# Kernel optimization log

Measured on AMD Instinct MI355X. Metric: run time of the kernel, lower is better.

## Reference

```python
import jax, jax.numpy as jnp
import numpy as np

N, D_IN, D_OUT, B = 200000, 256, 256, 256

def setup_inputs() -> dict:
    key = jax.random.key(0)
    k1, k2, k3, k4, k5 = jax.random.split(key, 5)
    lim = float(np.sqrt(6.0 / (D_IN + D_OUT)))  # xavier_init scale=1
    return {
        "nodes": jax.random.normal(k1, (N, D_IN), dtype=jnp.float32),
        "owner_masks": jax.random.randint(k2, (B, N), 0, 2, dtype=jnp.int32),
        "Wt": jax.random.uniform(k3, (D_OUT, D_IN), jnp.float32, -lim, lim),
        "bt": jax.random.normal(k4, (D_OUT,), dtype=jnp.float32),
        "Wg": jax.random.uniform(k5, (D_OUT, D_IN), jnp.float32, -lim, lim),
        "bg": jnp.ones((D_OUT,), dtype=jnp.float32),  # gate bias init fill_(1)
    }

def reference(nodes, owner_masks, Wt, bt, Wg, bg):
    # gates = sigmoid(Linear(nodes)); data = Linear(nodes)  -> [N, D_OUT]
    gates = jax.nn.sigmoid(nodes @ Wg.T + bg)
    data = nodes @ Wt.T + bt
    # owner-mask matmul == masked scatter-sum over nodes -> [B, D_OUT]
    fmask = owner_masks.astype(jnp.float32)
    res = jnp.einsum('bn,nd->bd', fmask, data * gates)
    return res  # dropout is identity in eval mode
```

## Files before the change

### kernel.cpp

```cpp
#include <hip/hip_runtime.h>
#include <stdint.h>

#define NND 200000

typedef unsigned short u16;
typedef __attribute__((ext_vector_type(4))) float f4;
typedef __attribute__((ext_vector_type(4))) int   i4;
typedef __attribute__((ext_vector_type(2))) unsigned int u2;
typedef __attribute__((ext_vector_type(8))) short s8;
typedef __attribute__((ext_vector_type(4))) float acc4;

__device__ __forceinline__ short f2bf(float f) {
    union { float f; uint32_t u; } v; v.f = f;
    uint32_t r = v.u + 0x7FFFu + ((v.u >> 16) & 1u);
    return (short)(r >> 16);
}
__device__ __forceinline__ uint32_t pack2bf(float a, float b) {
    uint32_t ua = __float_as_uint(a), ub = __float_as_uint(b);
    ua = ua + 0x7FFFu + ((ua >> 16) & 1u);
    ub = ub + 0x7FFFu + ((ub >> 16) & 1u);
    return (ua >> 16) | (ub & 0xFFFF0000u);
}
__device__ __forceinline__ float bf2f(uint32_t s) { return __uint_as_float(s << 16); }
__device__ __forceinline__ void gld16(const void* g, void* l) {
    __builtin_amdgcn_global_load_lds(
        (const __attribute__((address_space(1))) void*)g,
        (__attribute__((address_space(3))) void*)l, 16, 0, 0);
}

__global__ __launch_bounds__(256) void k_prep(const float* __restrict__ Wt,
                                              const float* __restrict__ Wg,
                                              u16* __restrict__ wtb,
                                              u16* __restrict__ wgb) {
    int i = blockIdx.x * 256 + threadIdx.x;
    wtb[i] = (u16)f2bf(Wt[i]);
    wgb[i] = (u16)f2bf(Wg[i]);
}

__global__ __launch_bounds__(512, 4) void k_h(const float* __restrict__ nodes,
                                              const u16* __restrict__ wtb,
                                              const u16* __restrict__ wgb,
                                              const float* __restrict__ btp,
                                              const float* __restrict__ bgp,
                                              u16* __restrict__ h_t) {
    __shared__ __align__(16) char smem[74752];
    u16* Abf = (u16*)smem;
    u16* Ws  = (u16*)(smem + 9216);
    u16* Hs  = (u16*)smem;

    const int tid  = threadIdx.x;
    const int lane = tid & 63, wave = tid >> 6;
    const int quad = lane >> 4, l16 = lane & 15;
    const int n0 = blockIdx.x * 64;
    const int arow = tid >> 3, aslot = tid & 7;

    acc4 at_[4][2], ag_[4][2];
#pragma unroll
    for (int rt = 0; rt < 4; ++rt)
#pragma unroll
        for (int dt = 0; dt < 2; ++dt) { at_[rt][dt] = (acc4)0.0f; ag_[rt][dt] = (acc4)0.0f; }

    for (int kt = 0; kt < 4; ++kt) {
        const int k0 = kt * 64;
        const float* ap = nodes + (size_t)(n0 + arow) * 256 + k0 + aslot * 8;
        f4 a0 = ((const f4*)ap)[0];
        f4 a1 = ((const f4*)ap)[1];
        if (kt) __syncthreads();
#pragma unroll
        for (int i = 0; i < 4; ++i) {
            int g = i * 512 + tid;
            int dr = g >> 3, c = g & 7;
            size_t off = (size_t)dr * 256 + k0 + ((c ^ (dr & 7)) << 3);
            gld16(wtb + off, (char*)Ws + g * 16);
            gld16(wgb + off, (char*)Ws + 32768 + g * 16);
        }
        {
            i4 aw;
            aw.x = (int)pack2bf(a0.x, a0.y); aw.y = (int)pack2bf(a0.z, a0.w);
            aw.z = (int)pack2bf(a1.x, a1.y); aw.w = (int)pack2bf(a1.z, a1.w);
            *(i4*)((char*)Abf + arow * 144 + ((aslot ^ (arow & 7)) << 4)) = aw;
        }
        __syncthreads();
#pragma unroll
        for (int ks = 0; ks < 2; ++ks) {
            const int q = (ks << 2) | quad;
            s8 af[4];
#pragma unroll
            for (int rt = 0; rt < 4; ++rt)
                af[rt] = *(const s8*)((char*)Abf + (rt * 16 + l16) * 144 + ((q ^ (l16 & 7)) << 4));
#pragma unroll
            for (int dt = 0; dt < 2; ++dt) {
                int dl = wave * 32 + dt * 16 + l16;
                int sl = (q ^ (dl & 7)) << 4;
                s8 bT = *(const s8*)((char*)Ws + dl * 128 + sl);
                s8 bG = *(const s8*)((char*)Ws + 32768 + dl * 128 + sl);
#pragma unroll
                for (int rt = 0; rt < 4; ++rt) {
                    at_[rt][dt] = __builtin_amdgcn_mfma_f32_16x16x32_bf16(af[rt], bT, at_[rt][dt], 0, 0, 0);
                    ag_[rt][dt] = __builtin_amdgcn_mfma_f32_16x16x32_bf16(af[rt], bG, ag_[rt][dt], 0, 0, 0);
                }
            }
        }
    }
    __syncthreads();

#pragma unroll
    for (int dt = 0; dt < 2; ++dt) {
        int dl = wave * 32 + dt * 16 + l16;
        float btv = btp[dl], bgv = bgp[dl];
#pragma unroll
        for (int rt = 0; rt < 4; ++rt) {
            float h0 = (at_[rt][dt][0] + btv) / (1.0f + __expf(-(ag_[rt][dt][0] + bgv)));
            float h1 = (at_[rt][dt][1] + btv) / (1.0f + __expf(-(ag_[rt][dt][1] + bgv)));
            float h2 = (at_[rt][dt][2] + btv) / (1.0f + __expf(-(ag_[rt][dt][2] + bgv)));
            float h3 = (at_[rt][dt][3] + btv) / (1.0f + __expf(-(ag_[rt][dt][3] + bgv)));
            u2 p; p.x = pack2bf(h0, h1); p.y = pack2bf(h2, h3);
            *(u2*)((char*)Hs + dl * 144 + (rt * 16 + quad * 4) * 2) = p;
        }
    }
    __syncthreads();
#pragma unroll
    for (int i = 0; i < 4; ++i) {
        int g = i * 512 + tid;
        int d = g >> 3, c = g & 7;
        f4 v = *(const f4*)((char*)Hs + d * 144 + c * 16);
        *(f4*)(h_t + (size_t)d * NND + n0 + c * 8) = v;
    }
}

__global__ __launch_bounds__(512, 4) void k_res(const int* __restrict__ masks,
                                                const u16* __restrict__ h_t,
                                                float* __restrict__ outp) {
    __shared__ __align__(16) char smem[49152];
    u16* Ms = (u16*)smem;
    u16* Hs = (u16*)(smem + 16384);

    const int tid  = threadIdx.x;
    const int lane = tid & 63, wave = tid >> 6;
    const int quad = lane >> 4, l16 = lane & 15;
    const int bh = wave & 1, dq = wave >> 1;
    const int b0 = blockIdx.x * 128;
    const int nbase = blockIdx.y * 960;
    const int R = min(15, (NND - nbase) / 64);

    acc4 acc[4][4];
#pragma unroll
    for (int rt = 0; rt < 4; ++rt)
#pragma unroll
        for (int dt = 0; dt < 4; ++dt) acc[rt][dt] = (acc4)0.0f;

    const int mr0 = tid >> 3, mc0 = tid & 7;
    const int mr1 = (512 + tid) >> 3, mc1 = tid & 7;
    i4 mp[2][2];
    {
        const i4* p0 = (const i4*)(masks + (size_t)(b0 + mr0) * NND + nbase + mc0 * 8);
        const i4* p1 = (const i4*)(masks + (size_t)(b0 + mr1) * NND + nbase + mc1 * 8);
        mp[0][0] = p0[0]; mp[0][1] = p0[1];
        mp[1][0] = p1[0]; mp[1][1] = p1[1];
    }

    for (int it = 0; it < R; ++it) {
        const int nb = nbase + it * 64;
#pragma unroll
        for (int i = 0; i < 4; ++i) {
            int g = i * 512 + tid;
            int dr = g >> 3, c = g & 7;
            gld16(h_t + (size_t)dr * NND + nb + ((c ^ (dr & 7)) << 3), (char*)Hs + g * 16);
        }
#pragma unroll
        for (int i = 0; i < 2; ++i) {
            int mr = (i == 0) ? mr0 : mr1, c = (i == 0) ? mc0 : mc1;
            i4 w;
            w.x = (int)((((uint32_t)(-mp[i][0].x)) & 0x3F80u) | ((((uint32_t)(-mp[i][0].y)) & 0x3F80u) << 16));
            w.y = (int)((((uint32_t)(-mp[i][0].z)) & 0x3F80u) | ((((uint32_t)(-mp[i][0].w)) & 0x3F80u) << 16));
            w.z = (int)((((uint32_t)(-mp[i][1].x)) & 0x3F80u) | ((((uint32_t)(-mp[i][1].y)) & 0x3F80u) << 16));
            w.w = (int)((((uint32_t)(-mp[i][1].z)) & 0x3F80u) | ((((uint32_t)(-mp[i][1].w)) & 0x3F80u) << 16));
            *(i4*)((char*)Ms + mr * 128 + ((c ^ (mr & 7)) << 4)) = w;
        }
        __syncthreads();
        if (it + 1 < R) {
            const int nn = nb + 64;
            const i4* p0 = (const i4*)(masks + (size_t)(b0 + mr0) * NND + nn + mc0 * 8);
            const i4* p1 = (const i4*)(masks + (size_t)(b0 + mr1) * NND + nn + mc1 * 8);
            mp[0][0] = p0[0]; mp[0][1] = p0[1];
            mp[1][0] = p1[0]; mp[1][1] = p1[1];
        }
#pragma unroll
        for (int ks = 0; ks < 2; ++ks) {
            const int q = (ks << 2) | quad;
            s8 af[4];
#pragma unroll
            for (int rt = 0; rt < 4; ++rt) {
                int r = bh * 64 + rt * 16 + l16;
                af[rt] = *(const s8*)((char*)Ms + r * 128 + ((q ^ (l16 & 7)) << 4));
            }
#pragma unroll
            for (int dt = 0; dt < 4; ++dt) {
                int dl = dq * 64 + dt * 16 + l16;
                s8 bf_ = *(const s8*)((char*)Hs + dl * 128 + ((q ^ (dl & 7)) << 4));
#pragma unroll
                for (int rt = 0; rt < 4; ++rt)
                    acc[rt][dt] = __builtin_amdgcn_mfma_f32_16x16x32_bf16(af[rt], bf_, acc[rt][dt], 0, 0, 0);
            }
        }
        __syncthreads();
    }
#pragma unroll
    for (int rt = 0; rt < 4; ++rt)
#pragma unroll
        for (int dt = 0; dt < 4; ++dt) {
            int b = b0 + bh * 64 + rt * 16 + quad * 4;
            int d = dq * 64 + dt * 16 + l16;
#pragma unroll
            for (int r = 0; r < 4; ++r)
                atomicAdd(outp + (size_t)(b + r) * 256 + d, acc[rt][dt][r]);
        }
}

extern "C" void kernel_launch(void* const* d_in, const int* in_sizes, int n_in,
                              void* d_out, int out_size, void* d_ws, size_t ws_size,
                              hipStream_t stream) {
    const float* nodes = (const float*)d_in[0];
    const int*   masks = (const int*)d_in[1];
    const float* Wt    = (const float*)d_in[2];
    const float* bt    = (const float*)d_in[3];
    const float* Wg    = (const float*)d_in[4];
    const float* bg    = (const float*)d_in[5];
    float* outp = (float*)d_out;

    u16* h_t = (u16*)d_ws;
    u16* wtb = (u16*)((char*)d_ws + (size_t)102400000);
    u16* wgb = wtb + 65536;

    hipMemsetAsync(d_out, 0, (size_t)out_size * sizeof(float), stream);
    k_prep<<<dim3(256), dim3(256), 0, stream>>>(Wt, Wg, wtb, wgb);
    k_h<<<dim3(3125), dim3(512), 0, stream>>>(nodes, wtb, wgb, bt, bg, h_t);
    k_res<<<dim3(2, 209), dim3(512), 0, stream>>>(masks, h_t, outp);
}
```

Baseline: 502.2 us.

## Make k_h persistent with register-resident weights and double-buffered node chunks

Rewrites the gated linear kernel so each 1024-thread block keeps its slice of both bf16 weight matrices in registers for its whole life. Each block then streams 25 chunks of 32 nodes through double-buffered LDS, prefetching the next chunk's inputs and writing out the previous chunk's results while the current chunk runs its MFMAs. This drops the per-block reload of the full weight matrices and shrinks the grid from 3125 blocks to 250, which risks lower occupancy (250 blocks against the number of CUs) and higher register pressure from holding the weights.

```diff
diff --git a/kernel.cpp b/kernel.cpp
--- a/kernel.cpp
+++ b/kernel.cpp
@@ -21,7 +21,6 @@
     ub = ub + 0x7FFFu + ((ub >> 16) & 1u);
     return (ua >> 16) | (ub & 0xFFFF0000u);
 }
-__device__ __forceinline__ float bf2f(uint32_t s) { return __uint_as_float(s << 16); }
 __device__ __forceinline__ void gld16(const void* g, void* l) {
     __builtin_amdgcn_global_load_lds(
         (const __attribute__((address_space(1))) void*)g,
@@ -37,94 +36,100 @@
     wgb[i] = (u16)f2bf(Wg[i]);
 }
 
-__global__ __launch_bounds__(512, 4) void k_h(const float* __restrict__ nodes,
-                                              const u16* __restrict__ wtb,
-                                              const u16* __restrict__ wgb,
-                                              const float* __restrict__ btp,
-                                              const float* __restrict__ bgp,
-                                              u16* __restrict__ h_t) {
-    __shared__ __align__(16) char smem[74752];
-    u16* Abf = (u16*)smem;
-    u16* Ws  = (u16*)(smem + 9216);
-    u16* Hs  = (u16*)smem;
+__global__ __launch_bounds__(1024, 4) void k_h(const float* __restrict__ nodes,
+                                               const u16* __restrict__ wtb,
+                                               const u16* __restrict__ wgb,
+                                               const float* __restrict__ btp,
+                                               const float* __restrict__ bgp,
+                                               u16* __restrict__ h_t) {
+    __shared__ __align__(16) char smem[69632];
+    char* A0 = smem;
+    char* A1 = smem + 16384;
+    char* H0 = smem + 32768;
+    char* H1 = smem + 51200;
 
     const int tid  = threadIdx.x;
     const int lane = tid & 63, wave = tid >> 6;
     const int quad = lane >> 4, l16 = lane & 15;
-    const int n0 = blockIdx.x * 64;
-    const int arow = tid >> 3, aslot = tid & 7;
-
-    acc4 at_[4][2], ag_[4][2];
-#pragma unroll
-    for (int rt = 0; rt < 4; ++rt)
-#pragma unroll
-        for (int dt = 0; dt < 2; ++dt) { at_[rt][dt] = (acc4)0.0f; ag_[rt][dt] = (acc4)0.0f; }
-
-    for (int kt = 0; kt < 4; ++kt) {
-        const int k0 = kt * 64;
-        const float* ap = nodes + (size_t)(n0 + arow) * 256 + k0 + aslot * 8;
-        f4 a0 = ((const f4*)ap)[0];
-        f4 a1 = ((const f4*)ap)[1];
-        if (kt) __syncthreads();
-#pragma unroll
-        for (int i = 0; i < 4; ++i) {
-            int g = i * 512 + tid;
-            int dr = g >> 3, c = g & 7;
-            size_t off = (size_t)dr * 256 + k0 + ((c ^ (dr & 7)) << 3);
-            gld16(wtb + off, (char*)Ws + g * 16);
-            gld16(wgb + off, (char*)Ws + 32768 + g * 16);
-        }
-        {
+    const int dgl  = wave * 16 + l16;
+
+    s8 wT[8], wG[8];
+    {
+        const u16* wtp = wtb + dgl * 256 + quad * 8;
+        const u16* wgp = wgb + dgl * 256 + quad * 8;
+#pragma unroll
+        for (int ks = 0; ks < 8; ++ks) {
+            wT[ks] = *(const s8*)(wtp + ks * 32);
+            wG[ks] = *(const s8*)(wgp + ks * 32);
+        }
+    }
+    const float btv = btp[dgl], bgv = bgp[dgl];
+
+    const int c0   = blockIdx.x * 25;
+    const int arow = tid >> 5, akq = tid & 31;
+    const int awbyte = akq * 512 + (((arow & 24) | ((arow ^ akq) & 7)) << 4);
+    const int sd = tid >> 2, sc = tid & 3;
+
+    f4 ar0, ar1;
+    {
+        const f4* p = (const f4*)(nodes + (size_t)(c0 * 32 + arow) * 256 + akq * 8);
+        ar0 = p[0]; ar1 = p[1];
+        i4 aw;
+        aw.x = (int)pack2bf(ar0.x, ar0.y); aw.y = (int)pack2bf(ar0.z, ar0.w);
+        aw.z = (int)pack2bf(ar1.x, ar1.y); aw.w = (int)pack2bf(ar1.z, ar1.w);
+        *(i4*)(A0 + awbyte) = aw;
+        const f4* q = (const f4*)(nodes + (size_t)((c0 + 1) * 32 + arow) * 256 + akq * 8);
+        ar0 = q[0]; ar1 = q[1];
+    }
+    __syncthreads();
+
+    char *Ard = A0, *Awr = A1, *Hwr = H0, *Hrd = H1;
+
+    for (int c = 0; c < 25; ++c) {
+        acc4 at0 = (acc4)0.0f, at1 = (acc4)0.0f, ag0 = (acc4)0.0f, ag1 = (acc4)0.0f;
+#pragma unroll
+        for (int ks = 0; ks < 8; ++ks) {
+            const int kq = ks * 4 + quad;
+            const int ab = kq * 512 + (((l16 & 8) | ((l16 ^ kq) & 7)) << 4);
+            s8 af0 = *(const s8*)(Ard + ab);
+            s8 af1 = *(const s8*)(Ard + ab + 256);
+            at0 = __builtin_amdgcn_mfma_f32_16x16x32_bf16(af0, wT[ks], at0, 0, 0, 0);
+            ag0 = __builtin_amdgcn_mfma_f32_16x16x32_bf16(af0, wG[ks], ag0, 0, 0, 0);
+            at1 = __builtin_amdgcn_mfma_f32_16x16x32_bf16(af1, wT[ks], at1, 0, 0, 0);
+            ag1 = __builtin_amdgcn_mfma_f32_16x16x32_bf16(af1, wG[ks], ag1, 0, 0, 0);
+        }
+        if (c < 24) {
             i4 aw;
-            aw.x = (int)pack2bf(a0.x, a0.y); aw.y = (int)pack2bf(a0.z, a0.w);
-            aw.z = (int)pack2bf(a1.x, a1.y); aw.w = (int)pack2bf(a1.z, a1.w);
-            *(i4*)((char*)Abf + arow * 144 + ((aslot ^ (arow & 7)) << 4)) = aw;
+            aw.x = (int)pack2bf(ar0.x, ar0.y); aw.y = (int)pack2bf(ar0.z, ar0.w);
+            aw.z = (int)pack2bf(ar1.x, ar1.y); aw.w = (int)pack2bf(ar1.z, ar1.w);
+            *(i4*)(Awr + awbyte) = aw;
+        }
+        if (c < 23) {
+            const f4* p = (const f4*)(nodes + (size_t)((c0 + c + 2) * 32 + arow) * 256 + akq * 8);
+            ar0 = p[0]; ar1 = p[1];
+        }
+#pragma unroll
+        for (int rt = 0; rt < 2; ++rt) {
+            const acc4 t = rt ? at1 : at0;
+            const acc4 g = rt ? ag1 : ag0;
+            float h0 = (t[0] + btv) / (1.0f + __expf(-(g[0] + bgv)));
+            float h1 = (t[1] + btv) / (1.0f + __expf(-(g[1] + bgv)));
+            float h2 = (t[2] + btv) / (1.0f + __expf(-(g[2] + bgv)));
+            float h3 = (t[3] + btv) / (1.0f + __expf(-(g[3] + bgv)));
+            u2 p; p.x = pack2bf(h0, h1); p.y = pack2bf(h2, h3);
+            *(u2*)(Hwr + dgl * 72 + rt * 32 + quad * 8) = p;
+        }
+        if (c > 0) {
+            f4 v = *(const f4*)(Hrd + sd * 72 + sc * 16);
+            *(f4*)(h_t + (size_t)sd * NND + (size_t)(c0 + c - 1) * 32 + sc * 8) = v;
         }
         __syncthreads();
-#pragma unroll
-        for (int ks = 0; ks < 2; ++ks) {
-            const int q = (ks << 2) | quad;
-            s8 af[4];
-#pragma unroll
-            for (int rt = 0; rt < 4; ++rt)
-                af[rt] = *(const s8*)((char*)Abf + (rt * 16 + l16) * 144 + ((q ^ (l16 & 7)) << 4));
-#pragma unroll
-            for (int dt = 0; dt < 2; ++dt) {
-                int dl = wave * 32 + dt * 16 + l16;
-                int sl = (q ^ (dl & 7)) << 4;
-                s8 bT = *(const s8*)((char*)Ws + dl * 128 + sl);
-                s8 bG = *(const s8*)((char*)Ws + 32768 + dl * 128 + sl);
-#pragma unroll
-                for (int rt = 0; rt < 4; ++rt) {
-                    at_[rt][dt] = __builtin_amdgcn_mfma_f32_16x16x32_bf16(af[rt], bT, at_[rt][dt], 0, 0, 0);
-                    ag_[rt][dt] = __builtin_amdgcn_mfma_f32_16x16x32_bf16(af[rt], bG, ag_[rt][dt], 0, 0, 0);
-                }
-            }
-        }
-    }
-    __syncthreads();
-
-#pragma unroll
-    for (int dt = 0; dt < 2; ++dt) {
-        int dl = wave * 32 + dt * 16 + l16;
-        float btv = btp[dl], bgv = bgp[dl];
-#pragma unroll
-        for (int rt = 0; rt < 4; ++rt) {
-            float h0 = (at_[rt][dt][0] + btv) / (1.0f + __expf(-(ag_[rt][dt][0] + bgv)));
-            float h1 = (at_[rt][dt][1] + btv) / (1.0f + __expf(-(ag_[rt][dt][1] + bgv)));
-            float h2 = (at_[rt][dt][2] + btv) / (1.0f + __expf(-(ag_[rt][dt][2] + bgv)));
-            float h3 = (at_[rt][dt][3] + btv) / (1.0f + __expf(-(ag_[rt][dt][3] + bgv)));
-            u2 p; p.x = pack2bf(h0, h1); p.y = pack2bf(h2, h3);
-            *(u2*)((char*)Hs + dl * 144 + (rt * 16 + quad * 4) * 2) = p;
-        }
-    }
-    __syncthreads();
-#pragma unroll
-    for (int i = 0; i < 4; ++i) {
-        int g = i * 512 + tid;
-        int d = g >> 3, c = g & 7;
-        f4 v = *(const f4*)((char*)Hs + d * 144 + c * 16);
-        *(f4*)(h_t + (size_t)d * NND + n0 + c * 8) = v;
+        char* tp = Ard; Ard = Awr; Awr = tp;
+        tp = Hwr; Hwr = Hrd; Hrd = tp;
+    }
+    {
+        f4 v = *(const f4*)(Hrd + sd * 72 + sc * 16);
+        *(f4*)(h_t + (size_t)sd * NND + (size_t)(c0 + 24) * 32 + sc * 8) = v;
     }
 }
 
@@ -234,6 +239,6 @@
 
     hipMemsetAsync(d_out, 0, (size_t)out_size * sizeof(float), stream);
     k_prep<<<dim3(256), dim3(256), 0, stream>>>(Wt, Wg, wtb, wgb);
-    k_h<<<dim3(3125), dim3(512), 0, stream>>>(nodes, wtb, wgb, bt, bg, h_t);
+    k_h<<<dim3(250), dim3(1024), 0, stream>>>(nodes, wtb, wgb, bt, bg, h_t);
     k_res<<<dim3(2, 209), dim3(512), 0, stream>>>(masks, h_t, outp);
 }
```

New measurement: 498.0 us. No clear change (-0.8%).
